# Kernel optimization log

Hardware: AMD Instinct MI355X
Metric: run time of the kernel (lower is better)

Reference implementation:

```python
import jax, jax.numpy as jnp
import numpy as np


def setup_inputs() -> dict:
    key = jax.random.key(0)
    k1, k2, k3, k4 = jax.random.split(key, 4)
    m, n, d = 1024, 1024, 2048  # d = 2 * hidden_dim, n = candidate_len
    u_p = jax.random.normal(k1, (m, d), dtype=jnp.float32)
    u_c = jax.random.normal(k2, (n, d), dtype=jnp.float32)
    # Linear(3*d, 1, bias=False) weight; scaled to keep softmax logits sane
    w_a = jax.random.normal(k3, (1, 3 * d), dtype=jnp.float32) * 0.02
    # Linear(4*d*n, 1) weight and bias
    ffn_w = jax.random.normal(k4, (1, 4 * d * n), dtype=jnp.float32) * 0.001
    ffn_b = jnp.zeros((1,), dtype=jnp.float32)
    return {"u_p": u_p, "u_c": u_c, "w_a": w_a, "ffn_w": ffn_w, "ffn_b": ffn_b}


def reference(u_p, u_c, w_a, ffn_w, ffn_b):
    m, d = u_p.shape
    n = u_c.shape[0]
    wa = w_a[0]  # [3d]
    w1, w2, w3 = wa[:d], wa[d:2 * d], wa[2 * d:]
    # s_ij = w_a . [u_p[i]; u_c[j]; u_p[i]*u_c[j]] decomposed into matmuls
    S = (u_p @ w1)[:, None] + (u_c @ w2)[None, :] + (u_p * w3) @ u_c.T  # [m, n]
    S_alpha = jax.nn.softmax(S, axis=1)      # [m, n], softmax over candidates
    S_beta = jax.nn.softmax(S.T, axis=1)     # [n, m], softmax over mentions
    # loop over k in range(n); with n <= m take first n rows where needed
    a_alpha = S_alpha[:n] @ u_c              # [n, d]
    a_beta = S_beta @ u_p                    # [n, d]
    X = jnp.concatenate(
        [u_p[:n], a_alpha, u_p[:n] * a_alpha, u_c * a_beta], axis=1
    ).reshape(-1)                            # [n * 4d]
    f = jax.nn.relu(X @ ffn_w.T + ffn_b)     # [1]
    return f
```

## Files before the change

### kernel.cpp

```cpp
#include <hip/hip_runtime.h>
#include <math.h>

#define TPB 256

typedef unsigned short u16;
typedef short bf16x8 __attribute__((ext_vector_type(8)));
typedef unsigned short u16x4 __attribute__((ext_vector_type(4)));
typedef float f32x4 __attribute__((ext_vector_type(4)));

__device__ __forceinline__ u16 f2bf(float x) {
    unsigned u = __float_as_uint(x);
    unsigned r = u + 0x7fffu + ((u >> 16) & 1u);
    return (u16)(r >> 16);
}
__device__ __forceinline__ float bf2f(u16 h) {
    return __uint_as_float(((unsigned)h) << 16);
}
__device__ __forceinline__ int pos32(int kk) {
    return ((kk >> 2) & 3) * 8 + (kk >> 4) * 4 + (kk & 3);
}
__device__ __forceinline__ int ipos32(int p5) {
    return 16 * ((p5 >> 2) & 1) + 4 * (p5 >> 3) + (p5 & 3);
}


#if defined(__has_builtin)
#if __has_builtin(__builtin_amdgcn_global_load_lds)
#define HAS_GLL 1
#endif
#endif
#ifndef HAS_GLL
#define HAS_GLL 0
#endif

__device__ __forceinline__ void gl16(const char* g, char* l) {
#if HAS_GLL
    __builtin_amdgcn_global_load_lds(
        (const __attribute__((address_space(1))) void*)(unsigned long long)g,
        (__attribute__((address_space(3))) void*)(unsigned int)(unsigned long long)l,
        16, 0, 0);
#else
    *(int4*)l = *(const int4*)g;
#endif
}

__global__ __launch_bounds__(TPB) void prep_kernel(
    const float* __restrict__ up, const float* __restrict__ uc,
    const float* __restrict__ wa, const float* __restrict__ W,
    u16* __restrict__ upw3, u16* __restrict__ ucb,
    u16* __restrict__ ucT, u16* __restrict__ upT,
    float* __restrict__ rpart, float* __restrict__ cpart,
    float* __restrict__ zbuf, float* __restrict__ fpart,
    int m, int n, int d, int nTc) {
    __shared__ float t[64 * 65];
    __shared__ float wred[4];
    int b = blockIdx.x, tid = threadIdx.x;
    if (b < 8) {
        int idx = b * TPB + tid;
        if (idx < 2 * m) zbuf[idx] = 0.f;
    }
    const float* src; u16* dstT; u16* dstR; float* bpart; int rows; int tt; int isUp;
    if (b < nTc) { src = uc; dstT = ucT; dstR = ucb;  bpart = cpart; rows = n; tt = b;       isUp = 0; }
    else         { src = up; dstT = upT; dstR = upw3; bpart = rpart; rows = m; tt = b - nTc; isUp = 1; }
    int ntx = d / 64;
    int c0 = (tt % ntx) * 64;
    int r0 = (tt / ntx) * 64;

    #pragma unroll
    for (int it = 0; it < 4; ++it) {
        int rr = (tid >> 4) + it * 16;
        int cc = (tid & 15) * 4;
        float4 v = *(const float4*)(src + (size_t)(r0 + rr) * d + c0 + cc);
        t[(cc + 0) * 65 + rr] = v.x;
        t[(cc + 1) * 65 + rr] = v.y;
        t[(cc + 2) * 65 + rr] = v.z;
        t[(cc + 3) * 65 + rr] = v.w;
    }
    __syncthreads();
    {
        char* tbase = (char*)dstT + (((size_t)(c0 >> 6) * (rows >> 6) + (r0 >> 6)) << 13);
        #pragma unroll
        for (int it = 0; it < 2; ++it) {
            int id = tid + it * TPB;
            int kc = id >> 3;
            int s = id & 7;
            u16 outv[8];
            #pragma unroll
            for (int e = 0; e < 8; ++e) {
                int p = s * 8 + e;
                int jloc = 32 * (p >> 5) + ipos32(p & 31);
                outv[e] = f2bf(t[kc * 65 + jloc]);
            }
            char* pp = tbase + kc * 128 + ((s * 16) ^ ((kc & 7) << 4));
            *(u16x4*)pp = *(u16x4*)&outv[0];
            *(u16x4*)(pp + 8) = *(u16x4*)&outv[4];
        }
    }
    {
        char* rbase = (char*)dstR + (((size_t)(r0 >> 6) * (d >> 6) + (c0 >> 6)) << 13);
        int rr = tid >> 2;
        int cbase = (tid & 3) * 16;
        #pragma unroll
        for (int grp = 0; grp < 4; ++grp) {
            int kl = cbase + grp * 4;
            u16x4 o;
            #pragma unroll
            for (int e = 0; e < 4; ++e) {
                float val = t[(kl + e) * 65 + rr];
                if (isUp) val *= wa[2 * d + c0 + kl + e];
                o[e] = f2bf(val);
            }
            int pl = (kl & ~31) + pos32(kl & 31);
            *(u16x4*)(rbase + rr * 128 + (((pl >> 3) << 4) ^ ((rr & 7) << 4)) + (pl & 7) * 2) = o;
        }
    }
    {
        int rr = tid >> 2;
        int kseg = tid & 3;
        const float* w = wa + (isUp ? 0 : d) + c0;
        float acc = 0.f;
        #pragma unroll
        for (int kk = 0; kk < 16; ++kk) {
            int k = kseg * 16 + kk;
            acc += t[k * 65 + rr] * w[k];
        }
        acc += __shfl_xor(acc, 1);
        acc += __shfl_xor(acc, 2);
        if (kseg == 0) bpart[(size_t)(c0 >> 6) * rows + r0 + rr] = acc;
    }
    if (isUp) {
        int rr = tid >> 2;
        int kseg = tid & 3;
        const float* w0r = W + (size_t)(r0 + rr) * 4 * d + c0 + kseg * 16;
        float acc = 0.f;
        #pragma unroll
        for (int kk = 0; kk < 16; ++kk) acc += t[(kseg * 16 + kk) * 65 + rr] * w0r[kk];
        #pragma unroll
        for (int off = 32; off > 0; off >>= 1) acc += __shfl_down(acc, off);
        if ((tid & 63) == 0) wred[tid >> 6] = acc;
        __syncthreads();
        if (tid == 0) fpart[tt] = wred[0] + wred[1] + wred[2] + wred[3];
    }
}

__global__ __launch_bounds__(TPB) void gemmS_mfma(
    const u16* __restrict__ Ah, const u16* __restrict__ Bh,
    u16* __restrict__ Sp, int m, int n, int d, int ksplit) {
    __shared__ u16 sA[128 * 64];
    __shared__ u16 sB[64 * 64];
    int tid = threadIdx.x;
    int lane = tid & 63, wave = tid >> 6;
    int wm = wave >> 1, wn = wave & 1;
    int lrow = lane & 15, g = lane >> 4;
    int by = blockIdx.y, bx = blockIdx.x;
    int i0 = by * 128, j0 = bx * 64;
    int ntk = d >> 6;
    int ktiles = ntk / ksplit;
    int tk0 = blockIdx.z * ktiles;
    u16* outS = Sp + (size_t)blockIdx.z * m * n;
    f32x4 acc[4][2];
    #pragma unroll
    for (int a = 0; a < 4; ++a)
        #pragma unroll
        for (int bq = 0; bq < 2; ++bq) acc[a][bq] = (f32x4){0.f, 0.f, 0.f, 0.f};

    int o = tid * 16;
    for (int tk = tk0; tk < tk0 + ktiles; ++tk) {
        const char* gA0 = (const char*)Ah + (((size_t)(2 * by) * ntk + tk) << 13);
        const char* gA1 = gA0 + ((size_t)ntk << 13);
        const char* gB = (const char*)Bh + (((size_t)bx * ntk + tk) << 13);
        gl16(gA0 + o, (char*)sA + o);
        gl16(gA0 + 4096 + o, (char*)sA + 4096 + o);
        gl16(gA1 + o, (char*)sA + 8192 + o);
        gl16(gA1 + 4096 + o, (char*)sA + 12288 + o);
        gl16(gB + o, (char*)sB + o);
        gl16(gB + 4096 + o, (char*)sB + 4096 + o);
        __syncthreads();
        #pragma unroll
        for (int kk = 0; kk < 2; ++kk) {
            bf16x8 af[4], bf[2];
            #pragma unroll
            for (int mr = 0; mr < 4; ++mr) {
                int row = wm * 64 + mr * 16 + lrow;
                int boff = (row * 128 + kk * 64 + g * 16) ^ ((row & 7) << 4);
                af[mr] = *(const bf16x8*)((const char*)sA + boff);
            }
            #pragma unroll
            for (int nr = 0; nr < 2; ++nr) {
                int row = wn * 32 + nr * 16 + lrow;
                int boff = (row * 128 + kk * 64 + g * 16) ^ ((row & 7) << 4);
                bf[nr] = *(const bf16x8*)((const char*)sB + boff);
            }
            #pragma unroll
            for (int mr = 0; mr < 4; ++mr)
                #pragma unroll
                for (int nr = 0; nr < 2; ++nr)
                    acc[mr][nr] = __builtin_amdgcn_mfma_f32_16x16x32_bf16(af[mr], bf[nr], acc[mr][nr], 0, 0, 0);
        }
        __syncthreads();
    }
    int crow = (lane >> 4) * 4;
    int ccol = lane & 15;
    #pragma unroll
    for (int mr = 0; mr < 4; ++mr)
        #pragma unroll
        for (int nr = 0; nr < 2; ++nr) {
            int jc = j0 + wn * 32 + nr * 16 + ccol;
            #pragma unroll
            for (int jr = 0; jr < 4; ++jr) {
                int i = i0 + wm * 64 + mr * 16 + crow + jr;
                outS[(size_t)i * n + jc] = f2bf(acc[mr][nr][jr]);
            }
        }
}

__global__ __launch_bounds__(TPB) void stats2_kernel(
    const u16* __restrict__ Sp, const float* __restrict__ rpart, const float* __restrict__ cpart,
    u16* __restrict__ E, u16* __restrict__ ET,
    float* __restrict__ rowsum, float* __restrict__ colsum,
    int m, int n) {
    __shared__ float t[64 * 65];
    __shared__ float rl[64], cl[64];
    int tid = threadIdx.x;
    int r0 = blockIdx.y * 64, c0 = blockIdx.x * 64;
    size_t mn = (size_t)m * n;
    int nkc = 32;
    if (tid < 64) {
        float a = 0.f;
        for (int kc = 0; kc < nkc; ++kc) a += rpart[(size_t)kc * m + r0 + tid];
        rl[tid] = a;
    } else if (tid < 128) {
        int j = tid - 64;
        float a = 0.f;
        for (int kc = 0; kc < nkc; ++kc) a += cpart[(size_t)kc * n + c0 + j];
        cl[j] = a;
    }
    __syncthreads();
    int row = tid >> 2, seg = tid & 3;
    size_t base = (size_t)(r0 + row) * n + c0 + seg * 16;
    float s[16];
    #pragma unroll
    for (int e = 0; e < 16; ++e) s[e] = 0.f;
    #pragma unroll
    for (int z = 0; z < 4; ++z) {
        const u16* sp = Sp + (size_t)z * mn + base;
        int4 q0 = *(const int4*)(sp);
        int4 q1 = *(const int4*)(sp + 8);
        const u16* p0 = (const u16*)&q0;
        const u16* p1 = (const u16*)&q1;
        #pragma unroll
        for (int e = 0; e < 8; ++e) { s[e] += bf2f(p0[e]); s[8 + e] += bf2f(p1[e]); }
    }
    float rv = rl[row];
    float racc = 0.f;
    u16 h[16];
    #pragma unroll
    for (int e = 0; e < 16; ++e) {
        int col = seg * 16 + e;
        float ex = __expf(s[e] + rv + cl[col]);
        h[e] = f2bf(ex);
        float er = bf2f(h[e]);
        racc += er;
        t[col * 65 + row] = er;
    }
    char* Ebase = (char*)E + (((size_t)(r0 >> 6) * (n >> 6) + (c0 >> 6)) << 13);
    #pragma unroll
    for (int g = 0; g < 4; ++g) {
        int cl4 = seg * 16 + g * 4;
        int pl = (cl4 & ~31) + pos32(cl4 & 31);
        *(u16x4*)(Ebase + row * 128 + (((pl >> 3) << 4) ^ ((row & 7) << 4)) + (pl & 7) * 2) = *(u16x4*)&h[g * 4];
    }
    racc += __shfl_xor(racc, 1);
    racc += __shfl_xor(racc, 2);
    if (seg == 0) unsafeAtomicAdd(rowsum + r0 + row, racc);
    __syncthreads();
    int col = tid >> 2, rseg = tid & 3;
    float cacc = 0.f;
    u16 hv[16];
    #pragma unroll
    for (int rr = 0; rr < 16; ++rr) {
        float val = t[col * 65 + rseg * 16 + rr];
        cacc += val;
        hv[rr] = f2bf(val);
    }
    cacc += __shfl_xor(cacc, 1);
    cacc += __shfl_xor(cacc, 2);
    if (rseg == 0) unsafeAtomicAdd(colsum + c0 + col, cacc);
    char* ETbase = (char*)ET + (((size_t)(c0 >> 6) * (m >> 6) + (r0 >> 6)) << 13);
    #pragma unroll
    for (int g = 0; g < 4; ++g) {
        int il = rseg * 16 + g * 4;
        int pl = (il & ~31) + pos32(il & 31);
        *(u16x4*)(ETbase + col * 128 + (((pl >> 3) << 4) ^ ((col & 7) << 4)) + (pl & 7) * 2) = *(u16x4*)&hv[g * 4];
    }
}

__global__ __launch_bounds__(TPB) void attn_mfma(
    const u16* __restrict__ E, const u16* __restrict__ ET,
    const u16* __restrict__ ucT, const u16* __restrict__ upT,
    const float* __restrict__ up, const float* __restrict__ uc,
    const float* __restrict__ W,
    const float* __restrict__ rowsum, const float* __restrict__ colsum,
    float* __restrict__ fpart2, int m, int n, int d) {
    __shared__ u16 sA[128 * 64];
    __shared__ u16 sB[64 * 64];
    __shared__ float red[TPB];
    int tid = threadIdx.x;
    int lane = tid & 63, wave = tid >> 6;
    int wm = wave >> 1, wn = wave & 1;
    int lrow = lane & 15, g = lane >> 4;
    int by = blockIdx.y, bx = blockIdx.x, bz = blockIdx.z;
    int i0 = by * 128, kc0 = bx * 64;
    const u16* A; const u16* B; const float* sums; int kT;
    if (bz == 0) { A = E;  B = ucT; sums = rowsum; kT = n; }
    else         { A = ET; B = upT; sums = colsum; kT = m; }
    int ntk = kT >> 6;
    f32x4 acc[4][2];
    #pragma unroll
    for (int a = 0; a < 4; ++a)
        #pragma unroll
        for (int bq = 0; bq < 2; ++bq) acc[a][bq] = (f32x4){0.f, 0.f, 0.f, 0.f};

    int o = tid * 16;
    for (int tj = 0; tj < ntk; ++tj) {
        const char* gA0 = (const char*)A + (((size_t)(2 * by) * ntk + tj) << 13);
        const char* gA1 = gA0 + ((size_t)ntk << 13);
        const char* gB = (const char*)B + (((size_t)bx * ntk + tj) << 13);
        gl16(gA0 + o, (char*)sA + o);
        gl16(gA0 + 4096 + o, (char*)sA + 4096 + o);
        gl16(gA1 + o, (char*)sA + 8192 + o);
        gl16(gA1 + 4096 + o, (char*)sA + 12288 + o);
        gl16(gB + o, (char*)sB + o);
        gl16(gB + 4096 + o, (char*)sB + 4096 + o);
        __syncthreads();
        #pragma unroll
        for (int kk = 0; kk < 2; ++kk) {
            bf16x8 af[4], bf[2];
            #pragma unroll
            for (int mr = 0; mr < 4; ++mr) {
                int row = wm * 64 + mr * 16 + lrow;
                int boff = (row * 128 + kk * 64 + g * 16) ^ ((row & 7) << 4);
                af[mr] = *(const bf16x8*)((const char*)sA + boff);
            }
            #pragma unroll
            for (int nr = 0; nr < 2; ++nr) {
                int row = wn * 32 + nr * 16 + lrow;
                int boff = (row * 128 + kk * 64 + g * 16) ^ ((row & 7) << 4);
                bf[nr] = *(const bf16x8*)((const char*)sB + boff);
            }
            #pragma unroll
            for (int mr = 0; mr < 4; ++mr)
                #pragma unroll
                for (int nr = 0; nr < 2; ++nr)
                    acc[mr][nr] = __builtin_amdgcn_mfma_f32_16x16x32_bf16(af[mr], bf[nr], acc[mr][nr], 0, 0, 0);
        }
        __syncthreads();
    }
    int crow = (lane >> 4) * 4;
    int ccol = lane & 15;
    float tsum = 0.f;
    if (bz == 0) {
        #pragma unroll
        for (int mr = 0; mr < 4; ++mr)
            #pragma unroll
            for (int jr = 0; jr < 4; ++jr) {
                int i = i0 + wm * 64 + mr * 16 + crow + jr;
                float inv = 1.f / sums[i];
                const float* wr = W + (size_t)i * 4 * d;
                const float* upr = up + (size_t)i * d;
                #pragma unroll
                for (int nr = 0; nr < 2; ++nr) {
                    int kc = kc0 + wn * 32 + nr * 16 + ccol;
                    float aa = acc[mr][nr][jr] * inv;
                    tsum += aa * (wr[d + kc] + upr[kc] * wr[2 * d + kc]);
                }
            }
    } else {
        #pragma unroll
        for (int mr = 0; mr < 4; ++mr)
            #pragma unroll
            for (int jr = 0; jr < 4; ++jr) {
                int j = i0 + wm * 64 + mr * 16 + crow + jr;
                float inv = 1.f / sums[j];
                const float* wr = W + (size_t)j * 4 * d;
                const float* ucr = uc + (size_t)j * d;
                #pragma unroll
                for (int nr = 0; nr < 2; ++nr) {
                    int kc = kc0 + wn * 32 + nr * 16 + ccol;
                    float ab = acc[mr][nr][jr] * inv;
                    tsum += ab * ucr[kc] * wr[3 * d + kc];
                }
            }
    }
    red[tid] = tsum;
    __syncthreads();
    for (int s = TPB / 2; s > 0; s >>= 1) {
        if (tid < s) red[tid] += red[tid + s];
        __syncthreads();
    }
    if (tid == 0)
        fpart2[(size_t)bz * gridDim.x * gridDim.y + (size_t)by * gridDim.x + bx] = red[0];
}

__global__ __launch_bounds__(TPB) void final_out(
    const float* __restrict__ fparts, int cnt, const float* __restrict__ bias,
    float* __restrict__ out) {
    __shared__ double red[TPB];
    double a = 0.0;
    for (int i = threadIdx.x; i < cnt; i += TPB) a += (double)fparts[i];
    red[threadIdx.x] = a;
    __syncthreads();
    for (int s = TPB / 2; s > 0; s >>= 1) {
        if (threadIdx.x < s) red[threadIdx.x] += red[threadIdx.x + s];
        __syncthreads();
    }
    if (threadIdx.x == 0) {
        double v = red[0] + (double)bias[0];
        out[0] = (float)(v > 0.0 ? v : 0.0);
    }
}

extern "C" void kernel_launch(void* const* d_in, const int* in_sizes, int n_in,
                              void* d_out, int out_size, void* d_ws, size_t ws_size,
                              hipStream_t stream) {
    const float* u_p = (const float*)d_in[0];
    const float* u_c = (const float*)d_in[1];
    const float* w_a = (const float*)d_in[2];
    const float* ffn_w = (const float*)d_in[3];
    const float* ffn_b = (const float*)d_in[4];
    float* out = (float*)d_out;

    int d = in_sizes[2] / 3;
    int m = in_sizes[0] / d;
    int n = in_sizes[1] / d;
    const int KSPLIT = 4;
    int nkc = d / 64;

    size_t md = (size_t)m * d, nd = (size_t)n * d, mn = (size_t)m * n;
    int nTc = (d / 64) * (n / 64);
    int nTp = (d / 64) * (m / 64);
    int nF2 = 2 * (d / 64) * (m / 128);

    float* ws = (float*)d_ws;
    float* rowsum = ws;
    float* colsum = rowsum + m;
    float* rpart = colsum + n;
    float* cpart = rpart + (size_t)nkc * m;
    float* fpart = cpart + (size_t)nkc * n;
    float* fpart2 = fpart + nTp;
    u16* Sp = (u16*)(fpart2 + nF2);
    u16* E = Sp + (size_t)KSPLIT * mn;
    u16* ET = E + mn;
    u16* upw3 = ET + mn;
    u16* ucb = upw3 + md;
    u16* ucT = ucb + nd;
    u16* upT = ucT + nd;

    prep_kernel<<<nTc + nTp, TPB, 0, stream>>>(
        u_p, u_c, w_a, ffn_w, upw3, ucb, ucT, upT, rpart, cpart, rowsum, fpart,
        m, n, d, nTc);

    dim3 gS(n / 64, m / 128, KSPLIT);
    gemmS_mfma<<<gS, TPB, 0, stream>>>(upw3, ucb, Sp, m, n, d, KSPLIT);

    dim3 gT(n / 64, m / 64);
    stats2_kernel<<<gT, TPB, 0, stream>>>(Sp, rpart, cpart, E, ET, rowsum, colsum, m, n);

    dim3 gA(d / 64, m / 128, 2);
    attn_mfma<<<gA, TPB, 0, stream>>>(E, ET, ucT, upT, u_p, u_c, ffn_w,
                                      rowsum, colsum, fpart2, m, n, d);

    final_out<<<1, TPB, 0, stream>>>(fpart, nTp + nF2, ffn_b, out);

    (void)out_size; (void)ws_size; (void)n_in;
}
```

Measured before the change: 55.28 us.

## Double-buffer LDS tiles in the S and attention MFMA GEMMs

Both the score GEMM and the attention GEMM now use two LDS buffers for their A and B tiles. The loads for the next k-tile are issued before the MFMA work on the current tile, with one barrier per iteration. The aim is to hide global-to-LDS load latency behind the matrix math instead of stalling on it every tile. In exchange, each block needs twice as much shared memory, about 48KB, which can lower the number of resident blocks per CU.

```diff
diff --git a/kernel.cpp b/kernel.cpp
--- a/kernel.cpp
+++ b/kernel.cpp
@@ -146,8 +146,8 @@
 __global__ __launch_bounds__(TPB) void gemmS_mfma(
     const u16* __restrict__ Ah, const u16* __restrict__ Bh,
     u16* __restrict__ Sp, int m, int n, int d, int ksplit) {
-    __shared__ u16 sA[128 * 64];
-    __shared__ u16 sB[64 * 64];
+    __shared__ u16 sA[2 * 128 * 64];
+    __shared__ u16 sB[2 * 64 * 64];
     int tid = threadIdx.x;
     int lane = tid & 63, wave = tid >> 6;
     int wm = wave >> 1, wn = wave & 1;
@@ -165,17 +165,27 @@
         for (int bq = 0; bq < 2; ++bq) acc[a][bq] = (f32x4){0.f, 0.f, 0.f, 0.f};
 
     int o = tid * 16;
-    for (int tk = tk0; tk < tk0 + ktiles; ++tk) {
+    auto stage = [&](int buf, int tk) {
         const char* gA0 = (const char*)Ah + (((size_t)(2 * by) * ntk + tk) << 13);
         const char* gA1 = gA0 + ((size_t)ntk << 13);
         const char* gB = (const char*)Bh + (((size_t)bx * ntk + tk) << 13);
-        gl16(gA0 + o, (char*)sA + o);
-        gl16(gA0 + 4096 + o, (char*)sA + 4096 + o);
-        gl16(gA1 + o, (char*)sA + 8192 + o);
-        gl16(gA1 + 4096 + o, (char*)sA + 12288 + o);
-        gl16(gB + o, (char*)sB + o);
-        gl16(gB + 4096 + o, (char*)sB + 4096 + o);
-        __syncthreads();
+        char* lA = (char*)sA + buf * 16384;
+        char* lB = (char*)sB + buf * 8192;
+        gl16(gA0 + o, lA + o);
+        gl16(gA0 + 4096 + o, lA + 4096 + o);
+        gl16(gA1 + o, lA + 8192 + o);
+        gl16(gA1 + 4096 + o, lA + 12288 + o);
+        gl16(gB + o, lB + o);
+        gl16(gB + 4096 + o, lB + 4096 + o);
+    };
+
+    stage(0, tk0);
+    __syncthreads();
+    int cur = 0;
+    for (int tk = tk0; tk < tk0 + ktiles; ++tk) {
+        if (tk + 1 < tk0 + ktiles) stage(cur ^ 1, tk + 1);
+        const char* lA = (const char*)sA + cur * 16384;
+        const char* lB = (const char*)sB + cur * 8192;
         #pragma unroll
         for (int kk = 0; kk < 2; ++kk) {
             bf16x8 af[4], bf[2];
@@ -183,13 +193,13 @@
             for (int mr = 0; mr < 4; ++mr) {
                 int row = wm * 64 + mr * 16 + lrow;
                 int boff = (row * 128 + kk * 64 + g * 16) ^ ((row & 7) << 4);
-                af[mr] = *(const bf16x8*)((const char*)sA + boff);
+                af[mr] = *(const bf16x8*)(lA + boff);
             }
             #pragma unroll
             for (int nr = 0; nr < 2; ++nr) {
                 int row = wn * 32 + nr * 16 + lrow;
                 int boff = (row * 128 + kk * 64 + g * 16) ^ ((row & 7) << 4);
-                bf[nr] = *(const bf16x8*)((const char*)sB + boff);
+                bf[nr] = *(const bf16x8*)(lB + boff);
             }
             #pragma unroll
             for (int mr = 0; mr < 4; ++mr)
@@ -198,6 +208,7 @@
                     acc[mr][nr] = __builtin_amdgcn_mfma_f32_16x16x32_bf16(af[mr], bf[nr], acc[mr][nr], 0, 0, 0);
         }
         __syncthreads();
+        cur ^= 1;
     }
     int crow = (lane >> 4) * 4;
     int ccol = lane & 15;
@@ -302,8 +313,8 @@
     const float* __restrict__ W,
     const float* __restrict__ rowsum, const float* __restrict__ colsum,
     float* __restrict__ fpart2, int m, int n, int d) {
-    __shared__ u16 sA[128 * 64];
-    __shared__ u16 sB[64 * 64];
+    __shared__ u16 sA[2 * 128 * 64];
+    __shared__ u16 sB[2 * 64 * 64];
     __shared__ float red[TPB];
     int tid = threadIdx.x;
     int lane = tid & 63, wave = tid >> 6;
@@ -322,17 +333,27 @@
         for (int bq = 0; bq < 2; ++bq) acc[a][bq] = (f32x4){0.f, 0.f, 0.f, 0.f};
 
     int o = tid * 16;
-    for (int tj = 0; tj < ntk; ++tj) {
+    auto stage = [&](int buf, int tj) {
         const char* gA0 = (const char*)A + (((size_t)(2 * by) * ntk + tj) << 13);
         const char* gA1 = gA0 + ((size_t)ntk << 13);
         const char* gB = (const char*)B + (((size_t)bx * ntk + tj) << 13);
-        gl16(gA0 + o, (char*)sA + o);
-        gl16(gA0 + 4096 + o, (char*)sA + 4096 + o);
-        gl16(gA1 + o, (char*)sA + 8192 + o);
-        gl16(gA1 + 4096 + o, (char*)sA + 12288 + o);
-        gl16(gB + o, (char*)sB + o);
-        gl16(gB + 4096 + o, (char*)sB + 4096 + o);
-        __syncthreads();
+        char* lA = (char*)sA + buf * 16384;
+        char* lB = (char*)sB + buf * 8192;
+        gl16(gA0 + o, lA + o);
+        gl16(gA0 + 4096 + o, lA + 4096 + o);
+        gl16(gA1 + o, lA + 8192 + o);
+        gl16(gA1 + 4096 + o, lA + 12288 + o);
+        gl16(gB + o, lB + o);
+        gl16(gB + 4096 + o, lB + 4096 + o);
+    };
+
+    stage(0, 0);
+    __syncthreads();
+    int cur = 0;
+    for (int tj = 0; tj < ntk; ++tj) {
+        if (tj + 1 < ntk) stage(cur ^ 1, tj + 1);
+        const char* lA = (const char*)sA + cur * 16384;
+        const char* lB = (const char*)sB + cur * 8192;
         #pragma unroll
         for (int kk = 0; kk < 2; ++kk) {
             bf16x8 af[4], bf[2];
@@ -340,13 +361,13 @@
             for (int mr = 0; mr < 4; ++mr) {
                 int row = wm * 64 + mr * 16 + lrow;
                 int boff = (row * 128 + kk * 64 + g * 16) ^ ((row & 7) << 4);
-                af[mr] = *(const bf16x8*)((const char*)sA + boff);
+                af[mr] = *(const bf16x8*)(lA + boff);
             }
             #pragma unroll
             for (int nr = 0; nr < 2; ++nr) {
                 int row = wn * 32 + nr * 16 + lrow;
                 int boff = (row * 128 + kk * 64 + g * 16) ^ ((row & 7) << 4);
-                bf[nr] = *(const bf16x8*)((const char*)sB + boff);
+                bf[nr] = *(const bf16x8*)(lB + boff);
             }
             #pragma unroll
             for (int mr = 0; mr < 4; ++mr)
@@ -355,6 +376,7 @@
                     acc[mr][nr] = __builtin_amdgcn_mfma_f32_16x16x32_bf16(af[mr], bf[nr], acc[mr][nr], 0, 0, 0);
         }
         __syncthreads();
+        cur ^= 1;
     }
     int crow = (lane >> 4) * 4;
     int ccol = lane & 15;
```

Result: faster. 51.45 us, median of 2 (-6.9%).
